# Performance work log

Hardware: AMD Instinct MI355X
Metric: run time of the kernel (lower is better)

The kernel has to match this reference:

```python
import jax, jax.numpy as jnp
import numpy as np

D_MODEL = 1024
NUM_HEADS = 16
HEAD_DIM = D_MODEL // NUM_HEADS
B, S = 2, 2048
EPS = 1e-8


def setup_inputs() -> dict:
    key = jax.random.key(0)
    ks = jax.random.split(key, 9)
    sc = 1.0 / np.sqrt(D_MODEL)
    return {
        "x": jax.random.normal(ks[0], (B, S, D_MODEL), jnp.float32),
        "wq": jax.random.normal(ks[1], (D_MODEL, D_MODEL), jnp.float32) * sc,
        "bq": jax.random.normal(ks[2], (D_MODEL,), jnp.float32) * 0.01,
        "wk": jax.random.normal(ks[3], (D_MODEL, D_MODEL), jnp.float32) * sc,
        "bk": jax.random.normal(ks[4], (D_MODEL,), jnp.float32) * 0.01,
        "wv": jax.random.normal(ks[5], (D_MODEL, D_MODEL), jnp.float32) * sc,
        "bv": jax.random.normal(ks[6], (D_MODEL,), jnp.float32) * 0.01,
        "wo": jax.random.normal(ks[7], (D_MODEL, D_MODEL), jnp.float32) * sc,
        "bo": jax.random.normal(ks[8], (D_MODEL,), jnp.float32) * 0.01,
    }


def reference(x, wq, bq, wk, bk, wv, bv, wo, bo):
    b, s, d = x.shape
    h, hd = NUM_HEADS, HEAD_DIM
    # projections (torch Linear: y = x W^T + b); reshape to [b, h, s, hd]
    def proj(w, bias):
        return (jnp.einsum('bsd,ed->bse', x, w) + bias).reshape(b, s, h, hd).transpose(0, 2, 1, 3)
    q = proj(wq, bq)
    k = proj(wk, bk)
    v = proj(wv, bv)
    scores = jnp.einsum('bhqd,bhkd->bhqk', q, k) / np.sqrt(hd)
    attn = jax.nn.softmax(scores, axis=-1)
    o = jnp.einsum('bhqk,bhkd->bhqd', attn, v)  # [b, h, s, hd]
    # per-position, per-head Gram-Schmidt exclusion: remove component of o[i]
    # along v[i] (the loop in the original is independent over positions)
    v_norm_sq = jnp.sum(v * v, axis=-1, keepdims=True)          # [b,h,s,1]
    align = jnp.sum(o * v, axis=-1, keepdims=True) / (v_norm_sq + EPS)
    o = o - align * v
    o = o.transpose(0, 2, 1, 3).reshape(b, s, d)
    return jnp.einsum('bsd,ed->bse', o, wo) + bo
```

## Files before the change

kernel.cpp:

```cpp
#include <hip/hip_runtime.h>
#include <stdint.h>

#define SEQ 2048
#define NTOK 4096
#define DM 1024

typedef __bf16 bf16x8 __attribute__((ext_vector_type(8)));
typedef __bf16 bf16x4 __attribute__((ext_vector_type(4)));
typedef float f32x4 __attribute__((ext_vector_type(4)));

__device__ __forceinline__ unsigned short f2bf(float f) {
  union { float f; unsigned u; } v; v.f = f;
  return (unsigned short)((v.u + 0x7fffu + ((v.u >> 16) & 1u)) >> 16);
}
__device__ __forceinline__ float bf2f(unsigned short s) {
  union { unsigned u; float f; } v; v.u = ((unsigned)s) << 16; return v.f;
}
__device__ __forceinline__ unsigned pkbf(float a, float b) {
  union { float f; unsigned u; } x, y; x.f = a; y.f = b;
  return __builtin_amdgcn_perm(y.u + 0x8000u, x.u + 0x8000u, 0x07060302u);
}

__device__ __forceinline__ void async16(const unsigned short* g, unsigned short* l) {
  __builtin_amdgcn_global_load_lds(
      (const __attribute__((address_space(1))) void*)g,
      (__attribute__((address_space(3))) void*)l, 16, 0, 0);
}

__global__ __launch_bounds__(256) void cast_all(
    const float* __restrict__ x, const float* __restrict__ wq,
    const float* __restrict__ wk, const float* __restrict__ wv,
    const float* __restrict__ wo, unsigned short* __restrict__ dst) {
  size_t i = ((size_t)blockIdx.x * 256 + threadIdx.x) * 4;
  const float* src; size_t off;
  if (i < (size_t)NTOK * DM) { src = x; off = i; }
  else {
    size_t j = i - (size_t)NTOK * DM;
    int s = (int)(j >> 20);
    src = (s == 0) ? wq : (s == 1) ? wk : (s == 2) ? wv : wo;
    off = j & 1048575u;
  }
  float4 f = *(const float4*)(src + off);
  ushort4 o;
  o.x = f2bf(f.x); o.y = f2bf(f.y); o.z = f2bf(f.z); o.w = f2bf(f.w);
  *(ushort4*)(dst + i) = o;
}


template<int MI>
__device__ __forceinline__ void stage_half(
    const unsigned short* __restrict__ A, const unsigned short* __restrict__ Bw,
    int m0, int n0, int kt, unsigned short* As, unsigned short* Bs) {
  const int tid = threadIdx.x;
  const int r = tid >> 2, c = tid & 3;
#pragma unroll
  for (int b = 0; b < MI / 2; ++b) {
    const int row = b * 64 + r;
    async16(A + (size_t)(m0 + row) * 1024 + kt + ((c ^ (row & 3)) << 3),
            As + row * 32 + c * 8);
  }
#pragma unroll
  for (int b = 0; b < 2; ++b) {
    const int row = b * 64 + r;
    async16(Bw + (size_t)(n0 + row) * 1024 + kt + ((c ^ (row & 3)) << 3),
            Bs + row * 32 + c * 8);
  }
}

__device__ __forceinline__ void pipe_bar0() {
  asm volatile("s_waitcnt vmcnt(0)\ns_barrier" ::: "memory");
}
template<int MI>
__device__ __forceinline__ void pipe_barN() {
  if constexpr (MI == 4) asm volatile("s_waitcnt vmcnt(4)\ns_barrier" ::: "memory");
  else                   asm volatile("s_waitcnt vmcnt(3)\ns_barrier" ::: "memory");
}

template<int MI>
__device__ __forceinline__ void gemm_pipe(
    const unsigned short* __restrict__ A, const unsigned short* __restrict__ Bw,
    int m0, int n0, f32x4 (&acc)[MI][4],
    unsigned short* AsBase, unsigned short* BsBase) {
  const int tid = threadIdx.x, lane = tid & 63, w = tid >> 6;
  const int wm16 = (w >> 1) * MI * 16, wn = (w & 1) * 64;
  const int quad = lane >> 4, l16 = lane & 15;
  constexpr int ASZ = MI * 32 * 32;
  constexpr int BSZ = 128 * 32;

  stage_half<MI>(A, Bw, m0, n0, 0,  AsBase,       BsBase);
  stage_half<MI>(A, Bw, m0, n0, 32, AsBase + ASZ, BsBase + BSZ);
  pipe_barN<MI>();

  int cur = 0;
  for (int p = 0; p < 32; ++p) {
    const unsigned short* As = AsBase + cur * ASZ;
    const unsigned short* Bs = BsBase + cur * BSZ;

    bf16x8 af[MI], bf[4];
    const int swz = ((quad ^ (l16 & 3)) << 3);
#pragma unroll
    for (int i = 0; i < MI; ++i)
      af[i] = *(const bf16x8*)(As + (wm16 + i * 16 + l16) * 32 + swz);
#pragma unroll
    for (int j = 0; j < 4; ++j)
      bf[j] = *(const bf16x8*)(Bs + (wn + j * 16 + l16) * 32 + swz);

    if (p + 2 < 32) {
      const int slot = (cur == 0) ? 2 : cur - 1;
      stage_half<MI>(A, Bw, m0, n0, (p + 2) * 32,
                     AsBase + slot * ASZ, BsBase + slot * BSZ);
    }

#pragma unroll
    for (int i = 0; i < MI; ++i)
#pragma unroll
      for (int j = 0; j < 4; ++j)
        acc[i][j] = __builtin_amdgcn_mfma_f32_16x16x32_bf16(af[i], bf[j], acc[i][j], 0, 0, 0);

    if (p < 30)       pipe_barN<MI>();
    else if (p == 30) pipe_bar0();
    cur = (cur == 2) ? 0 : cur + 1;
  }
}

__global__ __launch_bounds__(256, 3) void qkv_gemm(
    const unsigned short* __restrict__ xb,
    const unsigned short* __restrict__ wqb, const unsigned short* __restrict__ wkb,
    const unsigned short* __restrict__ wvb,
    const float* __restrict__ bq, const float* __restrict__ bk, const float* __restrict__ bv,
    unsigned short* __restrict__ Q, unsigned short* __restrict__ Kd,
    unsigned short* __restrict__ Vt) {
  __shared__ unsigned short As[3 * 128 * 32], Bs[3 * 128 * 32];
  const int gx = blockIdx.x;
  const int kind = gx >> 8;
  const int rr = gx & 255;
  const int tok = 4 * (rr & 7) + ((rr >> 3) & 3);
  const int oth = rr >> 5;
  const unsigned short* A; const unsigned short* Bw;
  int m0, n0;
  if (kind == 2) { A = wvb; Bw = xb; m0 = oth * 128; n0 = tok * 128; }
  else { A = xb; Bw = kind ? wkb : wqb; m0 = tok * 128; n0 = oth * 128; }

  f32x4 acc[4][4];
#pragma unroll
  for (int i = 0; i < 4; ++i)
#pragma unroll
    for (int j = 0; j < 4; ++j) { f32x4 z = {0.f, 0.f, 0.f, 0.f}; acc[i][j] = z; }
  gemm_pipe<4>(A, Bw, m0, n0, acc, As, Bs);

  const int lane = threadIdx.x & 63, w = threadIdx.x >> 6;
  const int quad = lane >> 4, l16 = lane & 15;
  const int wm = (w >> 1) * 64, wn = (w & 1) * 64;

  if (kind == 2) {
#pragma unroll
    for (int i = 0; i < 4; ++i)
#pragma unroll
      for (int j = 0; j < 4; ++j) {
        const int n = n0 + wn + j * 16 + l16;
        const int tb = n >> 11, s = n & 2047;
#pragma unroll
        for (int r = 0; r < 4; ++r) {
          const int m = m0 + wm + i * 16 + quad * 4 + r;
          const int h = m >> 6, d = m & 63;
          Vt[((size_t)(tb * 16 + h) * 64 + d) * SEQ + s] = f2bf(acc[i][j][r] + bv[m]);
        }
      }
  } else {
    const float* bias = (kind == 0) ? bq : bk;
    const float scale = (kind == 0) ? 0.180336880f : 1.0f;
#pragma unroll
    for (int i = 0; i < 4; ++i)
#pragma unroll
      for (int j = 0; j < 4; ++j) {
        const int col = n0 + wn + j * 16 + l16;
        const float bb = bias[col];
        const int h = col >> 6, d = col & 63;
#pragma unroll
        for (int r = 0; r < 4; ++r) {
          const int m = m0 + wm + i * 16 + quad * 4 + r;
          const int b = m >> 11, s = m & 2047;
          const int bh = b * 16 + h;
          const unsigned short val = f2bf((acc[i][j][r] + bb) * scale);
          if (kind == 0) Q[((size_t)bh * SEQ + s) * 64 + d] = val;
          else           Kd[((size_t)bh * SEQ + s) * 64 + d] = val;
        }
      }
  }
}

__global__ __launch_bounds__(256, 4) void attn_kernel(
    const unsigned short* __restrict__ Q, const unsigned short* __restrict__ Kd,
    const unsigned short* __restrict__ Vt,
    unsigned short* __restrict__ Op, float* __restrict__ Lp) {
  __shared__ unsigned short KV[4][4096];
  const int gx = blockIdx.x;
  const int xcd = gx & 7;
  const int idx = gx >> 3;
  const int bh  = xcd * 4 + (idx & 3);
  const int ksl = (idx >> 2) & 1;
  const int q0  = (idx >> 3) * 128;
  const int ks0 = ksl << 10;
  const int tid = threadIdx.x, lane = tid & 63, w = tid >> 6;
  const int quad = lane >> 4, l16 = lane & 15;
  const unsigned short* Qp = Q + (size_t)bh * SEQ * 64;
  const unsigned short* Kp = Kd + (size_t)bh * SEQ * 64;
  const unsigned short* Vp = Vt + (size_t)bh * 64 * SEQ;
  const int srow = tid >> 3;
  const int sc = ((tid & 7) ^ ((srow & 3) | ((srow & 8) >> 1))) << 3;

#pragma unroll
  for (int c = 0; c < 4; ++c)
    async16(Qp + (size_t)(q0 + c * 32 + srow) * 64 + sc,
            KV[c >> 1] + (c & 1) * 2048 + tid * 8);
  __syncthreads();

  const int gl = (l16 & 3) | ((l16 & 8) >> 1);
  const int sel = l16 & 7;
  const unsigned short* Qsrc = KV[w >> 1] + (w & 1) * 2048;
  bf16x8 bQ[2][2];
#pragma unroll
  for (int qq = 0; qq < 2; ++qq) {
    const int qrow = qq * 16 + l16;
#pragma unroll
    for (int hh = 0; hh < 2; ++hh)
      bQ[qq][hh] = *(const bf16x8*)(Qsrc + qrow * 64 + (((hh * 4 + quad) ^ gl) << 3));
  }
  __syncthreads();

  async16(Kp + (size_t)(ks0 + srow) * 64 + sc, KV[0] + tid * 8);
  async16(Kp + (size_t)(ks0 + 32 + srow) * 64 + sc, KV[0] + 2048 + tid * 8);
  async16(Vp + (size_t)srow * SEQ + ks0 + sc, KV[2] + tid * 8);
  async16(Vp + (size_t)(32 + srow) * SEQ + ks0 + sc, KV[2] + 2048 + tid * 8);

  union { unsigned short u[8]; bf16x8 v; } one8;
#pragma unroll
  for (int t = 0; t < 8; ++t) one8.u[t] = 0x3F80;
  const bf16x8 aOnes = one8.v;

  f32x4 o_acc[2][4];
  f32x4 l_acc[2];
  const f32x4 zinit = {-12.f, -12.f, -12.f, -12.f};
#pragma unroll
  for (int qq = 0; qq < 2; ++qq) {
    f32x4 z = {0.f, 0.f, 0.f, 0.f};
    l_acc[qq] = z;
#pragma unroll
    for (int dt = 0; dt < 4; ++dt) o_acc[qq][dt] = z;
  }

  for (int it = 0; it < 16; ++it) {
    const int cur = it & 1;
    __syncthreads();
    if (it + 1 < 16) {
      const int kt = ks0 + (it + 1) * 64, nb = (it + 1) & 1;
      async16(Kp + (size_t)(kt + srow) * 64 + sc, KV[nb] + tid * 8);
      async16(Kp + (size_t)(kt + 32 + srow) * 64 + sc, KV[nb] + 2048 + tid * 8);
      async16(Vp + (size_t)srow * SEQ + kt + sc, KV[2 + nb] + tid * 8);
      async16(Vp + (size_t)(32 + srow) * SEQ + kt + sc, KV[2 + nb] + 2048 + tid * 8);
    }
    const unsigned short* Ks = KV[cur];
    const unsigned short* Vs = KV[2 + cur];

    bf16x8 bP[2][2];
#pragma unroll
    for (int ee = 0; ee < 4; ++ee) {
      const int G = ee >> 1, e = ee & 1;
      const int R = G * 32 + ((l16 >> 2) << 3) + e * 4 + (l16 & 3);
      const unsigned short* arow = Ks + R * 64;
      bf16x8 a0 = *(const bf16x8*)(arow + ((quad ^ sel) << 3));
      bf16x8 a1 = *(const bf16x8*)(arow + (((4 + quad) ^ sel) << 3));
#pragma unroll
      for (int qq = 0; qq < 2; ++qq) {
        f32x4 z = __builtin_amdgcn_mfma_f32_16x16x32_bf16(a0, bQ[qq][0], zinit, 0, 0, 0);
        z = __builtin_amdgcn_mfma_f32_16x16x32_bf16(a1, bQ[qq][1], z, 0, 0, 0);
        const unsigned u0 = (unsigned)(int)__builtin_fmaf(z[0], 8388608.0f, 1065024977.0f);
        const unsigned u1 = (unsigned)(int)__builtin_fmaf(z[1], 8388608.0f, 1065024977.0f);
        const unsigned u2 = (unsigned)(int)__builtin_fmaf(z[2], 8388608.0f, 1065024977.0f);
        const unsigned u3 = (unsigned)(int)__builtin_fmaf(z[3], 8388608.0f, 1065024977.0f);
        union { unsigned d[4]; bf16x8 v; } pk;
        pk.v = bP[qq][G];
        pk.d[e * 2]     = __builtin_amdgcn_perm(u1, u0, 0x07060302u);
        pk.d[e * 2 + 1] = __builtin_amdgcn_perm(u3, u2, 0x07060302u);
        bP[qq][G] = pk.v;
      }
    }

#pragma unroll
    for (int qq = 0; qq < 2; ++qq)
#pragma unroll
      for (int G = 0; G < 2; ++G)
        l_acc[qq] = __builtin_amdgcn_mfma_f32_16x16x32_bf16(aOnes, bP[qq][G], l_acc[qq], 0, 0, 0);

#pragma unroll
    for (int dt = 0; dt < 4; ++dt) {
      const unsigned short* vbase = Vs + (dt * 16 + l16) * 64;
#pragma unroll
      for (int G = 0; G < 2; ++G) {
        bf16x8 aV = *(const bf16x8*)(vbase + (((G * 4 + quad) ^ gl) << 3));
#pragma unroll
        for (int qq = 0; qq < 2; ++qq)
          o_acc[qq][dt] = __builtin_amdgcn_mfma_f32_16x16x32_bf16(aV, bP[qq][G], o_acc[qq][dt], 0, 0, 0);
      }
    }
  }

  const size_t sb = (size_t)(ksl * 32 + bh);
#pragma unroll
  for (int qq = 0; qq < 2; ++qq) {
    const int qg = q0 + w * 32 + qq * 16 + l16;
#pragma unroll
    for (int dt = 0; dt < 4; ++dt)
#pragma unroll
      for (int r = 0; r < 4; ++r) {
        const int d = dt * 16 + quad * 4 + r;
        Op[(sb * 64 + d) * SEQ + qg] = f2bf(o_acc[qq][dt][r]);
      }
    if (quad == 0) Lp[sb * SEQ + qg] = l_acc[qq][0];
  }
}

__global__ __launch_bounds__(128) void combine_kernel(
    const unsigned short* __restrict__ Op, const float* __restrict__ Lp,
    const unsigned short* __restrict__ Vt, unsigned short* __restrict__ O) {
  const int bh = blockIdx.y;
  const int q = blockIdx.x * 128 + threadIdx.x;
  const size_t QC = (size_t)32 * SEQ;
  const size_t idx = (size_t)bh * SEQ + q;
  const float inv = 1.0f / (Lp[idx] + Lp[QC + idx]);
  const unsigned short* O1 = Op + (size_t)bh * 64 * SEQ + q;
  const unsigned short* O2 = O1 + QC * 64;
  const unsigned short* Vp = Vt + (size_t)bh * 64 * SEQ + q;
  float o64[64];
  float ov = 0.f, vv = 0.f;
#pragma unroll
  for (int d = 0; d < 64; ++d) {
    const float o = (bf2f(O1[(size_t)d * SEQ]) + bf2f(O2[(size_t)d * SEQ])) * inv;
    const float v = bf2f(Vp[(size_t)d * SEQ]);
    o64[d] = o; ov += o * v; vv += v * v;
  }
  const float align = ov / (vv + 1e-8f);
  const int b = bh >> 4, h = bh & 15;
  unsigned short* dst = O + (size_t)(b * SEQ + q) * DM + h * 64;
#pragma unroll
  for (int d = 0; d < 64; d += 2) {
    const float a0 = o64[d]     - align * bf2f(Vp[(size_t)d * SEQ]);
    const float a1 = o64[d + 1] - align * bf2f(Vp[(size_t)(d + 1) * SEQ]);
    *(unsigned*)(dst + d) = pkbf(a0, a1);
  }
}

__global__ __launch_bounds__(256, 3) void out_gemm(
    const unsigned short* __restrict__ Ob, const unsigned short* __restrict__ wob,
    const float* __restrict__ bo, float* __restrict__ out) {
  __shared__ unsigned short As[3 * 128 * 32], Bs[3 * 128 * 32];
  const int m0 = blockIdx.y * 128, n0 = blockIdx.x * 128;
  f32x4 acc[4][4];
#pragma unroll
  for (int i = 0; i < 4; ++i)
#pragma unroll
    for (int j = 0; j < 4; ++j) { f32x4 z = {0.f, 0.f, 0.f, 0.f}; acc[i][j] = z; }

  gemm_pipe<4>(Ob, wob, m0, n0, acc, As, Bs);

  const int lane = threadIdx.x & 63, w = threadIdx.x >> 6;
  const int quad = lane >> 4, l16 = lane & 15;
  const int wm = (w >> 1) * 64, wn = (w & 1) * 64;
#pragma unroll
  for (int i = 0; i < 4; ++i)
#pragma unroll
    for (int j = 0; j < 4; ++j) {
      const int col = n0 + wn + j * 16 + l16;
      const float bb = bo[col];
#pragma unroll
      for (int r = 0; r < 4; ++r) {
        const int m = m0 + wm + i * 16 + quad * 4 + r;
        out[(size_t)m * DM + col] = acc[i][j][r] + bb;
      }
    }
}

extern "C" void kernel_launch(void* const* d_in, const int* in_sizes, int n_in,
                              void* d_out, int out_size, void* d_ws, size_t ws_size,
                              hipStream_t stream) {
  const float* x  = (const float*)d_in[0];
  const float* wq = (const float*)d_in[1];
  const float* bq = (const float*)d_in[2];
  const float* wk = (const float*)d_in[3];
  const float* bk = (const float*)d_in[4];
  const float* wv = (const float*)d_in[5];
  const float* bv = (const float*)d_in[6];
  const float* wo = (const float*)d_in[7];
  const float* bo = (const float*)d_in[8];
  float* out = (float*)d_out;
  (void)in_sizes; (void)n_in; (void)out_size; (void)ws_size;

  unsigned short* ws  = (unsigned short*)d_ws;
  unsigned short* xb  = ws;
  unsigned short* wqb = xb + (size_t)NTOK * DM;
  unsigned short* wkb = wqb + (size_t)DM * DM;
  unsigned short* wvb = wkb + (size_t)DM * DM;
  unsigned short* wob = wvb + (size_t)DM * DM;
  unsigned short* Qb  = wob + (size_t)DM * DM;
  unsigned short* Kb  = Qb + (size_t)NTOK * DM;
  unsigned short* Vtb = Kb + (size_t)NTOK * DM;
  unsigned short* Ob  = Vtb + (size_t)NTOK * DM;
  unsigned short* Opb = Ob + (size_t)NTOK * DM;
  float* Lpw = (float*)(Opb + (size_t)2 * 32 * 64 * SEQ);

  cast_all<<<8192, 256, 0, stream>>>(x, wq, wk, wv, wo, ws);
  qkv_gemm<<<768, 256, 0, stream>>>(xb, wqb, wkb, wvb, bq, bk, bv, Qb, Kb, Vtb);
  attn_kernel<<<1024, 256, 0, stream>>>(Qb, Kb, Vtb, Opb, Lpw);
  combine_kernel<<<dim3(16, 32), 128, 0, stream>>>(Opb, Lpw, Vtb, Ob);
  out_gemm<<<dim3(8, 32), 256, 0, stream>>>(Ob, wob, bo, out);
}
```

Before: 186.9 us.

## Double attention query tile per block, raise MFMA priority, vectorize combine over two queries

Measured after the change: 183.0 us. -2.1%, faster.

```diff
diff --git a/kernel.cpp b/kernel.cpp
--- a/kernel.cpp
+++ b/kernel.cpp
@@ -189,7 +189,7 @@
   }
 }
 
-__global__ __launch_bounds__(256, 4) void attn_kernel(
+__global__ __launch_bounds__(256, 2) void attn_kernel(
     const unsigned short* __restrict__ Q, const unsigned short* __restrict__ Kd,
     const unsigned short* __restrict__ Vt,
     unsigned short* __restrict__ Op, float* __restrict__ Lp) {
@@ -199,7 +199,7 @@
   const int idx = gx >> 3;
   const int bh  = xcd * 4 + (idx & 3);
   const int ksl = (idx >> 2) & 1;
-  const int q0  = (idx >> 3) * 128;
+  const int q0  = (idx >> 3) * 256;
   const int ks0 = ksl << 10;
   const int tid = threadIdx.x, lane = tid & 63, w = tid >> 6;
   const int quad = lane >> 4, l16 = lane & 15;
@@ -210,17 +210,17 @@
   const int sc = ((tid & 7) ^ ((srow & 3) | ((srow & 8) >> 1))) << 3;
 
 #pragma unroll
-  for (int c = 0; c < 4; ++c)
+  for (int c = 0; c < 8; ++c)
     async16(Qp + (size_t)(q0 + c * 32 + srow) * 64 + sc,
             KV[c >> 1] + (c & 1) * 2048 + tid * 8);
   __syncthreads();
 
   const int gl = (l16 & 3) | ((l16 & 8) >> 1);
   const int sel = l16 & 7;
-  const unsigned short* Qsrc = KV[w >> 1] + (w & 1) * 2048;
-  bf16x8 bQ[2][2];
-#pragma unroll
-  for (int qq = 0; qq < 2; ++qq) {
+  const unsigned short* Qsrc = KV[w];
+  bf16x8 bQ[4][2];
+#pragma unroll
+  for (int qq = 0; qq < 4; ++qq) {
     const int qrow = qq * 16 + l16;
 #pragma unroll
     for (int hh = 0; hh < 2; ++hh)
@@ -238,11 +238,11 @@
   for (int t = 0; t < 8; ++t) one8.u[t] = 0x3F80;
   const bf16x8 aOnes = one8.v;
 
-  f32x4 o_acc[2][4];
-  f32x4 l_acc[2];
+  f32x4 o_acc[4][4];
+  f32x4 l_acc[4];
   const f32x4 zinit = {-12.f, -12.f, -12.f, -12.f};
 #pragma unroll
-  for (int qq = 0; qq < 2; ++qq) {
+  for (int qq = 0; qq < 4; ++qq) {
     f32x4 z = {0.f, 0.f, 0.f, 0.f};
     l_acc[qq] = z;
 #pragma unroll
@@ -262,7 +262,9 @@
     const unsigned short* Ks = KV[cur];
     const unsigned short* Vs = KV[2 + cur];
 
-    bf16x8 bP[2][2];
+    __builtin_amdgcn_s_setprio(1);
+
+    bf16x8 bP[4][2];
 #pragma unroll
     for (int ee = 0; ee < 4; ++ee) {
       const int G = ee >> 1, e = ee & 1;
@@ -271,7 +273,7 @@
       bf16x8 a0 = *(const bf16x8*)(arow + ((quad ^ sel) << 3));
       bf16x8 a1 = *(const bf16x8*)(arow + (((4 + quad) ^ sel) << 3));
 #pragma unroll
-      for (int qq = 0; qq < 2; ++qq) {
+      for (int qq = 0; qq < 4; ++qq) {
         f32x4 z = __builtin_amdgcn_mfma_f32_16x16x32_bf16(a0, bQ[qq][0], zinit, 0, 0, 0);
         z = __builtin_amdgcn_mfma_f32_16x16x32_bf16(a1, bQ[qq][1], z, 0, 0, 0);
         const unsigned u0 = (unsigned)(int)__builtin_fmaf(z[0], 8388608.0f, 1065024977.0f);
@@ -287,7 +289,7 @@
     }
 
 #pragma unroll
-    for (int qq = 0; qq < 2; ++qq)
+    for (int qq = 0; qq < 4; ++qq)
 #pragma unroll
       for (int G = 0; G < 2; ++G)
         l_acc[qq] = __builtin_amdgcn_mfma_f32_16x16x32_bf16(aOnes, bP[qq][G], l_acc[qq], 0, 0, 0);
@@ -299,16 +301,18 @@
       for (int G = 0; G < 2; ++G) {
         bf16x8 aV = *(const bf16x8*)(vbase + (((G * 4 + quad) ^ gl) << 3));
 #pragma unroll
-        for (int qq = 0; qq < 2; ++qq)
+        for (int qq = 0; qq < 4; ++qq)
           o_acc[qq][dt] = __builtin_amdgcn_mfma_f32_16x16x32_bf16(aV, bP[qq][G], o_acc[qq][dt], 0, 0, 0);
       }
     }
+
+    __builtin_amdgcn_s_setprio(0);
   }
 
   const size_t sb = (size_t)(ksl * 32 + bh);
 #pragma unroll
-  for (int qq = 0; qq < 2; ++qq) {
-    const int qg = q0 + w * 32 + qq * 16 + l16;
+  for (int qq = 0; qq < 4; ++qq) {
+    const int qg = q0 + w * 64 + qq * 16 + l16;
 #pragma unroll
     for (int dt = 0; dt < 4; ++dt)
 #pragma unroll
@@ -324,29 +328,44 @@
     const unsigned short* __restrict__ Op, const float* __restrict__ Lp,
     const unsigned short* __restrict__ Vt, unsigned short* __restrict__ O) {
   const int bh = blockIdx.y;
-  const int q = blockIdx.x * 128 + threadIdx.x;
+  const int q = (blockIdx.x * 128 + threadIdx.x) * 2;
   const size_t QC = (size_t)32 * SEQ;
   const size_t idx = (size_t)bh * SEQ + q;
-  const float inv = 1.0f / (Lp[idx] + Lp[QC + idx]);
+  const float inv0 = 1.0f / (Lp[idx] + Lp[QC + idx]);
+  const float inv1 = 1.0f / (Lp[idx + 1] + Lp[QC + idx + 1]);
   const unsigned short* O1 = Op + (size_t)bh * 64 * SEQ + q;
   const unsigned short* O2 = O1 + QC * 64;
   const unsigned short* Vp = Vt + (size_t)bh * 64 * SEQ + q;
-  float o64[64];
-  float ov = 0.f, vv = 0.f;
+  float oA[64], oB[64];
+  float ovA = 0.f, vvA = 0.f, ovB = 0.f, vvB = 0.f;
 #pragma unroll
   for (int d = 0; d < 64; ++d) {
-    const float o = (bf2f(O1[(size_t)d * SEQ]) + bf2f(O2[(size_t)d * SEQ])) * inv;
-    const float v = bf2f(Vp[(size_t)d * SEQ]);
-    o64[d] = o; ov += o * v; vv += v * v;
-  }
-  const float align = ov / (vv + 1e-8f);
+    const unsigned a = *(const unsigned*)(O1 + (size_t)d * SEQ);
+    const unsigned b = *(const unsigned*)(O2 + (size_t)d * SEQ);
+    const unsigned v = *(const unsigned*)(Vp + (size_t)d * SEQ);
+    const float o0 = (bf2f((unsigned short)a) + bf2f((unsigned short)b)) * inv0;
+    const float o1 = (bf2f((unsigned short)(a >> 16)) + bf2f((unsigned short)(b >> 16))) * inv1;
+    const float v0 = bf2f((unsigned short)v);
+    const float v1 = bf2f((unsigned short)(v >> 16));
+    oA[d] = o0; oB[d] = o1;
+    ovA += o0 * v0; vvA += v0 * v0;
+    ovB += o1 * v1; vvB += v1 * v1;
+  }
+  const float alA = ovA / (vvA + 1e-8f);
+  const float alB = ovB / (vvB + 1e-8f);
   const int b = bh >> 4, h = bh & 15;
-  unsigned short* dst = O + (size_t)(b * SEQ + q) * DM + h * 64;
+  unsigned short* dst0 = O + (size_t)(b * SEQ + q) * DM + h * 64;
+  unsigned short* dst1 = dst0 + DM;
 #pragma unroll
   for (int d = 0; d < 64; d += 2) {
-    const float a0 = o64[d]     - align * bf2f(Vp[(size_t)d * SEQ]);
-    const float a1 = o64[d + 1] - align * bf2f(Vp[(size_t)(d + 1) * SEQ]);
-    *(unsigned*)(dst + d) = pkbf(a0, a1);
+    const unsigned va = *(const unsigned*)(Vp + (size_t)d * SEQ);
+    const unsigned vb = *(const unsigned*)(Vp + (size_t)(d + 1) * SEQ);
+    const float a0 = oA[d]     - alA * bf2f((unsigned short)va);
+    const float a1 = oA[d + 1] - alA * bf2f((unsigned short)vb);
+    const float b0 = oB[d]     - alB * bf2f((unsigned short)(va >> 16));
+    const float b1 = oB[d + 1] - alB * bf2f((unsigned short)(vb >> 16));
+    *(unsigned*)(dst0 + d) = pkbf(a0, a1);
+    *(unsigned*)(dst1 + d) = pkbf(b0, b1);
   }
 }
 
@@ -410,7 +429,7 @@
 
   cast_all<<<8192, 256, 0, stream>>>(x, wq, wk, wv, wo, ws);
   qkv_gemm<<<768, 256, 0, stream>>>(xb, wqb, wkb, wvb, bq, bk, bv, Qb, Kb, Vtb);
-  attn_kernel<<<1024, 256, 0, stream>>>(Qb, Kb, Vtb, Opb, Lpw);
-  combine_kernel<<<dim3(16, 32), 128, 0, stream>>>(Opb, Lpw, Vtb, Ob);
+  attn_kernel<<<512, 256, 0, stream>>>(Qb, Kb, Vtb, Opb, Lpw);
+  combine_kernel<<<dim3(8, 32), 128, 0, stream>>>(Opb, Lpw, Vtb, Ob);
   out_gemm<<<dim3(8, 32), 256, 0, stream>>>(Ob, wob, bo, out);
 }
```

## Drop split-K attention and fuse normalization and Gram-Schmidt epilogue into attention kernel

Applied to the files above, without the earlier changes.

After: 181.4 us. 1.03x faster.

```diff
diff --git a/kernel.cpp b/kernel.cpp
--- a/kernel.cpp
+++ b/kernel.cpp
@@ -192,15 +192,13 @@
 __global__ __launch_bounds__(256, 4) void attn_kernel(
     const unsigned short* __restrict__ Q, const unsigned short* __restrict__ Kd,
     const unsigned short* __restrict__ Vt,
-    unsigned short* __restrict__ Op, float* __restrict__ Lp) {
+    unsigned short* __restrict__ O) {
   __shared__ unsigned short KV[4][4096];
   const int gx = blockIdx.x;
   const int xcd = gx & 7;
   const int idx = gx >> 3;
   const int bh  = xcd * 4 + (idx & 3);
-  const int ksl = (idx >> 2) & 1;
-  const int q0  = (idx >> 3) * 128;
-  const int ks0 = ksl << 10;
+  const int q0  = (idx >> 2) * 128;
   const int tid = threadIdx.x, lane = tid & 63, w = tid >> 6;
   const int quad = lane >> 4, l16 = lane & 15;
   const unsigned short* Qp = Q + (size_t)bh * SEQ * 64;
@@ -228,10 +226,10 @@
   }
   __syncthreads();
 
-  async16(Kp + (size_t)(ks0 + srow) * 64 + sc, KV[0] + tid * 8);
-  async16(Kp + (size_t)(ks0 + 32 + srow) * 64 + sc, KV[0] + 2048 + tid * 8);
-  async16(Vp + (size_t)srow * SEQ + ks0 + sc, KV[2] + tid * 8);
-  async16(Vp + (size_t)(32 + srow) * SEQ + ks0 + sc, KV[2] + 2048 + tid * 8);
+  async16(Kp + (size_t)srow * 64 + sc, KV[0] + tid * 8);
+  async16(Kp + (size_t)(32 + srow) * 64 + sc, KV[0] + 2048 + tid * 8);
+  async16(Vp + (size_t)srow * SEQ + sc, KV[2] + tid * 8);
+  async16(Vp + (size_t)(32 + srow) * SEQ + sc, KV[2] + 2048 + tid * 8);
 
   union { unsigned short u[8]; bf16x8 v; } one8;
 #pragma unroll
@@ -249,11 +247,11 @@
     for (int dt = 0; dt < 4; ++dt) o_acc[qq][dt] = z;
   }
 
-  for (int it = 0; it < 16; ++it) {
+  for (int it = 0; it < 32; ++it) {
     const int cur = it & 1;
     __syncthreads();
-    if (it + 1 < 16) {
-      const int kt = ks0 + (it + 1) * 64, nb = (it + 1) & 1;
+    if (it + 1 < 32) {
+      const int kt = (it + 1) * 64, nb = (it + 1) & 1;
       async16(Kp + (size_t)(kt + srow) * 64 + sc, KV[nb] + tid * 8);
       async16(Kp + (size_t)(kt + 32 + srow) * 64 + sc, KV[nb] + 2048 + tid * 8);
       async16(Vp + (size_t)srow * SEQ + kt + sc, KV[2 + nb] + tid * 8);
@@ -261,6 +259,8 @@
     }
     const unsigned short* Ks = KV[cur];
     const unsigned short* Vs = KV[2 + cur];
+
+    __builtin_amdgcn_s_setprio(1);
 
     bf16x8 bP[2][2];
 #pragma unroll
@@ -303,50 +303,45 @@
           o_acc[qq][dt] = __builtin_amdgcn_mfma_f32_16x16x32_bf16(aV, bP[qq][G], o_acc[qq][dt], 0, 0, 0);
       }
     }
-  }
-
-  const size_t sb = (size_t)(ksl * 32 + bh);
+
+    __builtin_amdgcn_s_setprio(0);
+  }
+
+  const int b = bh >> 4, h = bh & 15;
 #pragma unroll
   for (int qq = 0; qq < 2; ++qq) {
     const int qg = q0 + w * 32 + qq * 16 + l16;
+    const float inv = 1.0f / l_acc[qq][0];
+    const unsigned short* vp = Vp + qg;
+    float ov = 0.f, v2 = 0.f;
 #pragma unroll
     for (int dt = 0; dt < 4; ++dt)
 #pragma unroll
       for (int r = 0; r < 4; ++r) {
         const int d = dt * 16 + quad * 4 + r;
-        Op[(sb * 64 + d) * SEQ + qg] = f2bf(o_acc[qq][dt][r]);
-      }
-    if (quad == 0) Lp[sb * SEQ + qg] = l_acc[qq][0];
-  }
-}
-
-__global__ __launch_bounds__(128) void combine_kernel(
-    const unsigned short* __restrict__ Op, const float* __restrict__ Lp,
-    const unsigned short* __restrict__ Vt, unsigned short* __restrict__ O) {
-  const int bh = blockIdx.y;
-  const int q = blockIdx.x * 128 + threadIdx.x;
-  const size_t QC = (size_t)32 * SEQ;
-  const size_t idx = (size_t)bh * SEQ + q;
-  const float inv = 1.0f / (Lp[idx] + Lp[QC + idx]);
-  const unsigned short* O1 = Op + (size_t)bh * 64 * SEQ + q;
-  const unsigned short* O2 = O1 + QC * 64;
-  const unsigned short* Vp = Vt + (size_t)bh * 64 * SEQ + q;
-  float o64[64];
-  float ov = 0.f, vv = 0.f;
-#pragma unroll
-  for (int d = 0; d < 64; ++d) {
-    const float o = (bf2f(O1[(size_t)d * SEQ]) + bf2f(O2[(size_t)d * SEQ])) * inv;
-    const float v = bf2f(Vp[(size_t)d * SEQ]);
-    o64[d] = o; ov += o * v; vv += v * v;
-  }
-  const float align = ov / (vv + 1e-8f);
-  const int b = bh >> 4, h = bh & 15;
-  unsigned short* dst = O + (size_t)(b * SEQ + q) * DM + h * 64;
-#pragma unroll
-  for (int d = 0; d < 64; d += 2) {
-    const float a0 = o64[d]     - align * bf2f(Vp[(size_t)d * SEQ]);
-    const float a1 = o64[d + 1] - align * bf2f(Vp[(size_t)(d + 1) * SEQ]);
-    *(unsigned*)(dst + d) = pkbf(a0, a1);
+        const float v = bf2f(vp[(size_t)d * SEQ]);
+        ov += o_acc[qq][dt][r] * v;
+        v2 += v * v;
+      }
+    ov *= inv;
+    ov += __shfl_xor(ov, 16); ov += __shfl_xor(ov, 32);
+    v2 += __shfl_xor(v2, 16); v2 += __shfl_xor(v2, 32);
+    const float align = ov / (v2 + 1e-8f);
+    unsigned short* dst = O + (size_t)(b * SEQ + qg) * DM + h * 64;
+#pragma unroll
+    for (int dt = 0; dt < 4; ++dt) {
+      float a[4];
+#pragma unroll
+      for (int r = 0; r < 4; ++r) {
+        const int d = dt * 16 + quad * 4 + r;
+        const float v = bf2f(vp[(size_t)d * SEQ]);
+        a[r] = __builtin_fmaf(o_acc[qq][dt][r], inv, -align * v);
+      }
+      uint2 pk2;
+      pk2.x = pkbf(a[0], a[1]);
+      pk2.y = pkbf(a[2], a[3]);
+      *(uint2*)(dst + dt * 16 + quad * 4) = pk2;
+    }
   }
 }
 
@@ -405,12 +400,9 @@
   unsigned short* Kb  = Qb + (size_t)NTOK * DM;
   unsigned short* Vtb = Kb + (size_t)NTOK * DM;
   unsigned short* Ob  = Vtb + (size_t)NTOK * DM;
-  unsigned short* Opb = Ob + (size_t)NTOK * DM;
-  float* Lpw = (float*)(Opb + (size_t)2 * 32 * 64 * SEQ);
 
   cast_all<<<8192, 256, 0, stream>>>(x, wq, wk, wv, wo, ws);
   qkv_gemm<<<768, 256, 0, stream>>>(xb, wqb, wkb, wvb, bq, bk, bv, Qb, Kb, Vtb);
-  attn_kernel<<<1024, 256, 0, stream>>>(Qb, Kb, Vtb, Opb, Lpw);
-  combine_kernel<<<dim3(16, 32), 128, 0, stream>>>(Opb, Lpw, Vtb, Ob);
+  attn_kernel<<<512, 256, 0, stream>>>(Qb, Kb, Vtb, Ob);
   out_gemm<<<dim3(8, 32), 256, 0, stream>>>(Ob, wob, bo, out);
 }
```
